# Optimization experiments

Measured on AMD Instinct MI355X. Metric: run time of the kernel, lower is better.

The kernel has to match this reference:

```python
import jax, jax.numpy as jnp
import numpy as np


def setup_inputs() -> dict:
    key = jax.random.key(0)
    ks = jax.random.split(key, 5)
    B, C, H, W = 4, 256, 48, 48
    x = jax.random.normal(ks[0], (B, C, H, W), dtype=jnp.float32)
    w_qkv = jax.random.normal(ks[1], (3 * C, C), dtype=jnp.float32) * (C ** -0.5)
    b_qkv = jax.random.normal(ks[2], (3 * C,), dtype=jnp.float32) * 0.02
    w_proj = jax.random.normal(ks[3], (C, C), dtype=jnp.float32) * (C ** -0.5)
    b_proj = jax.random.normal(ks[4], (C,), dtype=jnp.float32) * 0.02
    return {"x": x, "w_qkv": w_qkv, "b_qkv": b_qkv, "w_proj": w_proj, "b_proj": b_proj, "num_heads": 4}


def reference(x, w_qkv, b_qkv, w_proj, b_proj, num_heads):
    B, C, H, W = x.shape
    N = H * W
    hd = C // num_heads
    # NOTE: original uses full-dim scale, not head_dim
    scale = C ** -0.5
    # 1x1 conv == channel matmul
    qkv = jnp.einsum('bchw,oc->bohw', x, w_qkv) + b_qkv[None, :, None, None]
    qkv = qkv.reshape(B, 3, num_heads, hd, N)
    q = qkv[:, 0].transpose(0, 1, 3, 2)  # [B, h, N, d]
    k = qkv[:, 1]                         # [B, h, d, N]
    v = qkv[:, 2].transpose(0, 1, 3, 2)  # [B, h, N, d]
    attn = jax.nn.softmax((q @ k) * scale, axis=-1)  # [B, h, N, N]
    out = attn @ v                        # [B, h, N, d]
    out = out.transpose(0, 1, 3, 2).reshape(B, C, H, W)
    return jnp.einsum('bchw,oc->bohw', out, w_proj) + b_proj[None, :, None, None]
```

## Files before the change

kernel.cpp:

```cpp
#include <hip/hip_runtime.h>
#include <hip/hip_bf16.h>
#include <stdint.h>

typedef unsigned short u16;
typedef unsigned int u32;
typedef __attribute__((ext_vector_type(8))) short bf16x8;
typedef __attribute__((ext_vector_type(4))) short bf16x4;
typedef __attribute__((ext_vector_type(4))) float f32x4;
typedef __attribute__((ext_vector_type(2))) unsigned int u32x2;
typedef __attribute__((ext_vector_type(4))) unsigned short u16x4;

#define MFMA16 __builtin_amdgcn_mfma_f32_16x16x32_bf16

#if __has_builtin(__builtin_amdgcn_mfma_f32_16x16x16bf16_1k)
__device__ __forceinline__ f32x4 MFMAK16(u32x2 a, u32x2 b, f32x4 c) {
  return __builtin_amdgcn_mfma_f32_16x16x16bf16_1k(
      __builtin_bit_cast(bf16x4, a), __builtin_bit_cast(bf16x4, b), c, 0, 0, 0);
}
#elif __has_builtin(__builtin_amdgcn_mfma_f32_16x16x16_bf16)
typedef __attribute__((ext_vector_type(4))) __bf16 bf16v4;
__device__ __forceinline__ f32x4 MFMAK16(u32x2 a, u32x2 b, f32x4 c) {
  return __builtin_amdgcn_mfma_f32_16x16x16_bf16(
      __builtin_bit_cast(bf16v4, a), __builtin_bit_cast(bf16v4, b), c, 0, 0, 0);
}
#else
__device__ __forceinline__ f32x4 MFMAK16(u32x2 a, u32x2 b, f32x4 c) {
  f32x4 d;
  asm("s_nop 1\n\tv_mfma_f32_16x16x16_bf16 %0, %1, %2, %3"
      : "=v"(d) : "v"(a), "v"(b), "v"(c));
  return d;
}
#endif

static constexpr int Bb = 4;
static constexpr int Cc = 256;
static constexpr int NHh = 4;
static constexpr int HDd = 64;
static constexpr int Nn = 2304;
static constexpr int NSPLIT = 6;

__device__ __forceinline__ u16 f2bf(float f) {
  u32 u = __builtin_bit_cast(u32, f);
  u32 r = u + 0x7fffu + ((u >> 16) & 1u);
  return (u16)(r >> 16);
}

__device__ __forceinline__ u32 cvtpk(float a, float b) {
  u32 r;
  asm("v_cvt_pk_bf16_f32 %0, %1, %2" : "=v"(r) : "v"(a), "v"(b));
  return r;
}

__device__ __forceinline__ float blo(u32 u) { return __builtin_bit_cast(float, u << 16); }
__device__ __forceinline__ float bhi(u32 u) { return __builtin_bit_cast(float, u & 0xffff0000u); }

__device__ __forceinline__ void async16(const void* g, void* l) {
  __builtin_amdgcn_global_load_lds(
      (const __attribute__((address_space(1))) u32*)g,
      (__attribute__((address_space(3))) u32*)l, 16, 0, 0);
}

__global__ __launch_bounds__(256) void k_prep(const float* __restrict__ wq,
                                              const float* __restrict__ wp,
                                              u16* __restrict__ wqb,
                                              u16* __restrict__ wpb) {
  int i = blockIdx.x * 256 + threadIdx.x;
  if (i < 3 * Cc * Cc) wqb[i] = f2bf(wq[i]);
  if (i < Cc * Cc)     wpb[i] = f2bf(wp[i]);
}

__global__ __launch_bounds__(256) void k_qkv(const u16* __restrict__ wqb,
                                             const float* __restrict__ x,
                                             const float* __restrict__ bqkv,
                                             u16* __restrict__ qT, u16* __restrict__ kT,
                                             u16* __restrict__ vT) {
  __shared__ float tile[64][65];
  __shared__ u16 Bs[64 * 256];
  int n0 = blockIdx.y * 64, b = blockIdx.z;
  int t = threadIdx.x, w = t >> 6, l = t & 63, g = l >> 4, li = l & 15;
  char* BsB = (char*)Bs;
#pragma unroll
  for (int cc = 0; cc < 4; ++cc) {
#pragma unroll
    for (int i = 0; i < 16; ++i) {
      int cl = i * 4 + w;
      tile[cl][l] = x[((size_t)(b * Cc + cc * 64 + cl)) * Nn + n0 + l];
    }
    __syncthreads();
#pragma unroll
    for (int i = 0; i < 16; ++i) {
      int nr = i * 4 + w;
      int byte = nr * 512 + ((2 * (cc * 64 + l)) ^ ((nr & 7) << 4));
      *(u16*)(BsB + byte) = f2bf(tile[l][nr]);
    }
    __syncthreads();
  }
  const float qs = 0.0625f * 1.44269504088896340736f;
#pragma unroll
  for (int p = 0; p < 2; ++p) {
    int o0 = blockIdx.x * 128 + p * 64;
    const u16* Arow = wqb + (size_t)(o0 + w * 16 + li) * Cc;
    f32x4 acc[4] = {};
#pragma unroll
    for (int s = 0; s < 8; ++s) {
      bf16x8 a = *(const bf16x8*)(Arow + s * 32 + g * 8);
#pragma unroll
      for (int nt = 0; nt < 4; ++nt) {
        int row = nt * 16 + li;
        const char* bp_ = (const char*)Bs + row * 512 + ((s * 64 + g * 16) ^ ((row & 7) << 4));
        bf16x8 bb = *(const bf16x8*)bp_;
        acc[nt] = MFMA16(a, bb, acc[nt], 0, 0, 0);
      }
    }
    int which = o0 >> 8;
    int hh = (o0 >> 6) & 3;
    int bh = b * NHh + hh;
    int dbase = w * 16 + g * 4;
#pragma unroll
    for (int nt = 0; nt < 4; ++nt) {
      int n = n0 + nt * 16 + li;
      float v0 = acc[nt][0] + bqkv[o0 + dbase + 0];
      float v1 = acc[nt][1] + bqkv[o0 + dbase + 1];
      float v2 = acc[nt][2] + bqkv[o0 + dbase + 2];
      float v3 = acc[nt][3] + bqkv[o0 + dbase + 3];
      if (which == 0) {
        u16x4 pq = {f2bf(v0 * qs), f2bf(v1 * qs), f2bf(v2 * qs), f2bf(v3 * qs)};
        *(u16x4*)(qT + ((size_t)bh * Nn + n) * HDd + dbase) = pq;
      } else if (which == 1) {
        u16x4 pk = {f2bf(v0), f2bf(v1), f2bf(v2), f2bf(v3)};
        *(u16x4*)(kT + ((size_t)bh * Nn + n) * HDd + dbase) = pk;
      } else {
        vT[((size_t)bh * HDd + dbase + 0) * Nn + n] = f2bf(v0);
        vT[((size_t)bh * HDd + dbase + 1) * Nn + n] = f2bf(v1);
        vT[((size_t)bh * HDd + dbase + 2) * Nn + n] = f2bf(v2);
        vT[((size_t)bh * HDd + dbase + 3) * Nn + n] = f2bf(v3);
      }
    }
  }
}

__global__ __launch_bounds__(192) void k_attn(const u16* __restrict__ qT,
                                              const u16* __restrict__ kT,
                                              const u16* __restrict__ vT,
                                              u16* __restrict__ attP,
                                              float* __restrict__ lsumP) {
  __shared__ u16 Ks[2][32 * 64];
  __shared__ u16 Vs[2][64 * 32];
  int L = blockIdx.x;
  int xcd = L & 7, r2 = L >> 3;
  int bh = 2 * xcd + (r2 >= 144 ? 1 : 0);
  int rr = (r2 >= 144) ? r2 - 144 : r2;
  int sext = rr / 24;
  int qb = rr % 24;
  int t = threadIdx.x, w = t / 64, l = t & 63, g = l >> 4, li = l & 15;
  int q0 = qb * 96 + w * 32;
  const u16* qr0 = qT + ((size_t)bh * Nn + q0 + li) * HDd;
  const u16* qr1 = qT + ((size_t)bh * Nn + q0 + 16 + li) * HDd;
  bf16x8 bq[2][2];
  bq[0][0] = *(const bf16x8*)(qr0 + g * 8);
  bq[0][1] = *(const bf16x8*)(qr0 + 32 + g * 8);
  bq[1][0] = *(const bf16x8*)(qr1 + g * 8);
  bq[1][1] = *(const bf16x8*)(qr1 + 32 + g * 8);
  const u32 one2 = 0x3F803F80u;
  u32x2 ONESK = {one2, one2};
  f32x4 acc[2][4] = {};
  f32x4 acc_l[2] = {};
  const char* kbh = (const char*)(kT + (size_t)bh * Nn * HDd);
  const char* vbh = (const char*)(vT + (size_t)bh * HDd * Nn);
  int sw_li = (li & 7) << 4;
  int sw2   = ((li >> 1) & 3) << 4;

  const char* sp[3];
  int sd[3];
  ptrdiff_t sstr[3];
  bool son[3], svv[3];
#pragma unroll
  for (int it = 0; it < 3; ++it) {
    int gg = w * 3 + it;
    son[it] = (gg < 8);
    int c = gg * 64 + l;
    if (c < 256) {
      int key = c >> 3, c8 = c & 7;
      sp[it] = kbh + (size_t)(sext * 384 + key) * 128 + ((c8 * 16) ^ ((key & 7) << 4));
      sd[it] = c * 16; sstr[it] = 32 * 128; svv[it] = false;
    } else {
      int cv = c - 256, d = cv >> 2, c4 = cv & 3;
      sp[it] = vbh + (size_t)d * (Nn * 2) + sext * 768 +
               ((c4 * 16) ^ (((d >> 1) & 3) << 4));
      sd[it] = cv * 16; sstr[it] = 32 * 2; svv[it] = true;
    }
  }

  auto STAGE = [&](int buf) {
    char* kdst = (char*)(&Ks[0][0]) + buf * 4096;
    char* vdst = (char*)(&Vs[0][0]) + buf * 4096;
#pragma unroll
    for (int it = 0; it < 3; ++it) {
      if (son[it]) {
        async16(sp[it], (svv[it] ? vdst : kdst) + sd[it]);
        sp[it] += sstr[it];
      }
    }
  };

  STAGE(0);
  int cur = 0;
  for (int kb = 0; kb < 12; ++kb) {
    __syncthreads();
    if (kb + 1 < 12) STAGE(cur ^ 1);

    const char* Kc = (const char*)(&Ks[0][0]) + cur * 4096;
    const char* Vc = (const char*)(&Vs[0][0]) + cur * 4096;

    f32x4 s[2][2];
    __builtin_amdgcn_s_setprio(1);
#pragma unroll
    for (int kt = 0; kt < 2; ++kt) {
      const char* kr = Kc + (kt * 16 + li) * 128;
      bf16x8 a0 = *(const bf16x8*)(kr + ((g * 16) ^ sw_li));
      bf16x8 a1 = *(const bf16x8*)(kr + ((64 + g * 16) ^ sw_li));
#pragma unroll
      for (int st = 0; st < 2; ++st) {
        f32x4 z = {};
        z = MFMA16(a0, bq[st][0], z, 0, 0, 0);
        z = MFMA16(a1, bq[st][1], z, 0, 0, 0);
        s[st][kt] = z;
      }
    }
    __builtin_amdgcn_s_setprio(0);

    u32x2 pb[2][2];
#pragma unroll
    for (int st = 0; st < 2; ++st)
#pragma unroll
      for (int kt = 0; kt < 2; ++kt) {
#pragma unroll
        for (int j = 0; j < 4; ++j) s[st][kt][j] = exp2f(s[st][kt][j]);
        pb[st][kt][0] = cvtpk(s[st][kt][0], s[st][kt][1]);
        pb[st][kt][1] = cvtpk(s[st][kt][2], s[st][kt][3]);
      }

    __builtin_amdgcn_s_setprio(1);
    acc_l[0] = MFMAK16(ONESK, pb[0][0], acc_l[0]);
    acc_l[0] = MFMAK16(ONESK, pb[0][1], acc_l[0]);
    acc_l[1] = MFMAK16(ONESK, pb[1][0], acc_l[1]);
    acc_l[1] = MFMAK16(ONESK, pb[1][1], acc_l[1]);
#pragma unroll
    for (int dt = 0; dt < 4; ++dt) {
      const char* vr = Vc + (dt * 16 + li) * 64;
#pragma unroll
      for (int kt = 0; kt < 2; ++kt) {
        u32x2 vf = *(const u32x2*)(vr + ((kt * 32 + g * 8) ^ sw2));
        acc[0][dt] = MFMAK16(vf, pb[0][kt], acc[0][dt]);
        acc[1][dt] = MFMAK16(vf, pb[1][kt], acc[1][dt]);
      }
    }
    __builtin_amdgcn_s_setprio(0);
    cur ^= 1;
  }
  asm volatile("s_nop 7\n\ts_nop 7");
  u16* ap = attP + (size_t)sext * (Bb * Nn * Cc);
  float* lp = lsumP + sext * (Bb * NHh * Nn);
  if (l < 16) {
    lp[bh * Nn + q0 + li] = acc_l[0][0];
    lp[bh * Nn + q0 + 16 + li] = acc_l[1][0];
  }
  int b = bh >> 2, hh = bh & 3;
#pragma unroll
  for (int st = 0; st < 2; ++st) {
    int q = q0 + st * 16 + li;
#pragma unroll
    for (int dt = 0; dt < 4; ++dt) {
      u16x4 pk = {f2bf(acc[st][dt][0]), f2bf(acc[st][dt][1]),
                  f2bf(acc[st][dt][2]), f2bf(acc[st][dt][3])};
      *(u16x4*)(ap + ((size_t)(b * Nn + q)) * Cc + hh * 64 + dt * 16 + g * 4) = pk;
    }
  }
}

__global__ __launch_bounds__(256) void k_merge(const u16* __restrict__ attP,
                                               const float* __restrict__ lsumP,
                                               u16* __restrict__ attT) {
  int gid = blockIdx.x * 256 + threadIdx.x;
  int base = gid * 8;
  int bidx = base / (Nn * Cc);
  int rem = base - bidx * (Nn * Cc);
  int n = rem >> 8, c = rem & 255;
  int hh = c >> 6;
  int lidx = (bidx * NHh + hh) * Nn + n;
  const int LQ = Bb * NHh * Nn;
  float lsum = 0.f;
#pragma unroll
  for (int q = 0; q < NSPLIT; ++q) lsum += lsumP[q * LQ + lidx];
  float inv = 1.0f / lsum;
  const size_t QSZ = (size_t)Bb * Nn * Cc;
  float s0 = 0, s1 = 0, s2 = 0, s3 = 0, s4 = 0, s5 = 0, s6 = 0, s7 = 0;
#pragma unroll
  for (int q = 0; q < NSPLIT; ++q) {
    uint4 p = *(const uint4*)(attP + q * QSZ + base);
    s0 += blo(p.x); s1 += bhi(p.x);
    s2 += blo(p.y); s3 += bhi(p.y);
    s4 += blo(p.z); s5 += bhi(p.z);
    s6 += blo(p.w); s7 += bhi(p.w);
  }
  uint4 o;
  o.x = cvtpk(s0 * inv, s1 * inv);
  o.y = cvtpk(s2 * inv, s3 * inv);
  o.z = cvtpk(s4 * inv, s5 * inv);
  o.w = cvtpk(s6 * inv, s7 * inv);
  *(uint4*)(attT + base) = o;
}

__global__ __launch_bounds__(256) void k_proj(const u16* __restrict__ wpb,
                                              const u16* __restrict__ attT,
                                              const float* __restrict__ bp,
                                              float* __restrict__ out) {
  __shared__ u16 Bs[32 * 256];
  int bx = blockIdx.x, n0 = blockIdx.y * 32, b = blockIdx.z;
  int t = threadIdx.x, w = t >> 6, l = t & 63, g = l >> 4, li = l & 15;
#pragma unroll
  for (int it = 0; it < 4; ++it) {
    int ch = it * 256 + t;
    int row = ch >> 5, c16 = ch & 31;
    const char* src = (const char*)attT + ((size_t)(b * Nn + n0 + row)) * 512 +
                      ((c16 * 16) ^ ((row & 7) << 4));
    async16(src, (char*)Bs + (it * 256 + (t & ~63)) * 16);
  }
  const u16* Arow0 = wpb + (size_t)(bx * 128 + w * 16 + li) * Cc;
  const u16* Arow1 = Arow0 + (size_t)64 * Cc;
  __syncthreads();
  f32x4 acc[2][2] = {};
#pragma unroll
  for (int s = 0; s < 8; ++s) {
    bf16x8 a0 = *(const bf16x8*)(Arow0 + s * 32 + g * 8);
    bf16x8 a1 = *(const bf16x8*)(Arow1 + s * 32 + g * 8);
#pragma unroll
    for (int nt = 0; nt < 2; ++nt) {
      int row = nt * 16 + li;
      const char* bp_ = (const char*)Bs + row * 512 + ((s * 64 + g * 16) ^ ((row & 7) << 4));
      bf16x8 bb = *(const bf16x8*)bp_;
      acc[0][nt] = MFMA16(a0, bb, acc[0][nt], 0, 0, 0);
      acc[1][nt] = MFMA16(a1, bb, acc[1][nt], 0, 0, 0);
    }
  }
#pragma unroll
  for (int nt = 0; nt < 2; ++nt) {
    int n = n0 + nt * 16 + li;
#pragma unroll
    for (int p = 0; p < 2; ++p) {
      int obase = bx * 128 + p * 64 + w * 16 + g * 4;
#pragma unroll
      for (int j = 0; j < 4; ++j) {
        out[((size_t)(b * Cc + obase + j)) * Nn + n] = acc[p][nt][j] + bp[obase + j];
      }
    }
  }
}

extern "C" void kernel_launch(void* const* d_in, const int* in_sizes, int n_in,
                              void* d_out, int out_size, void* d_ws, size_t ws_size,
                              hipStream_t stream) {
  const float* x     = (const float*)d_in[0];
  const float* wqkv  = (const float*)d_in[1];
  const float* bqkv  = (const float*)d_in[2];
  const float* wproj = (const float*)d_in[3];
  const float* bproj = (const float*)d_in[4];
  float* out = (float*)d_out;

  u16* ws    = (u16*)d_ws;
  u16* wq_bf = ws;
  u16* wp_bf = wq_bf + 196608;
  u16* qT    = wp_bf + 65536;
  u16* kT    = qT + 2359296;
  u16* vT    = kT + 2359296;
  u16* attP  = vT + 2359296;
  float* lsumP = (float*)(attP + NSPLIT * 2359296);
  u16* attT  = qT;

  k_prep<<<dim3(768), dim3(256), 0, stream>>>(wqkv, wproj, wq_bf, wp_bf);
  k_qkv<<<dim3(6, 36, 4), dim3(256), 0, stream>>>(wq_bf, x, bqkv, qT, kT, vT);
  k_attn<<<dim3(2304), dim3(192), 0, stream>>>(qT, kT, vT, attP, lsumP);
  k_merge<<<dim3(1152), dim3(256), 0, stream>>>(attP, lsumP, attT);
  k_proj<<<dim3(2, 72, 4), dim3(256), 0, stream>>>(wp_bf, attT, bproj, out);
}
```

Measured before the change: 90.72 us.

## Halve key-split count and double attention key tile to 64 keys

Splits each head's keys into 3 chunks instead of 6 and stages 64-key K/V tiles per iteration instead of 32, with a new V swizzle. This halves the number of attention blocks, the partial-output writes, and the merge traffic, and each block does more MFMA work per barrier. The costs are doubled LDS use per block, more registers for the larger P tile, and fewer blocks in flight, which may reduce occupancy and latency hiding.

```diff
diff --git a/kernel.cpp b/kernel.cpp
--- a/kernel.cpp
+++ b/kernel.cpp
@@ -37,7 +37,7 @@
 static constexpr int NHh = 4;
 static constexpr int HDd = 64;
 static constexpr int Nn = 2304;
-static constexpr int NSPLIT = 6;
+static constexpr int NSPLIT = 3;
 
 __device__ __forceinline__ u16 f2bf(float f) {
   u32 u = __builtin_bit_cast(u32, f);
@@ -144,12 +144,12 @@
                                               const u16* __restrict__ vT,
                                               u16* __restrict__ attP,
                                               float* __restrict__ lsumP) {
-  __shared__ u16 Ks[2][32 * 64];
-  __shared__ u16 Vs[2][64 * 32];
+  __shared__ u16 Ks[2][64 * 64];
+  __shared__ u16 Vs[2][64 * 64];
   int L = blockIdx.x;
   int xcd = L & 7, r2 = L >> 3;
-  int bh = 2 * xcd + (r2 >= 144 ? 1 : 0);
-  int rr = (r2 >= 144) ? r2 - 144 : r2;
+  int bh = 2 * xcd + (r2 >= 72 ? 1 : 0);
+  int rr = (r2 >= 72) ? r2 - 72 : r2;
   int sext = rr / 24;
   int qb = rr % 24;
   int t = threadIdx.x, w = t / 64, l = t & 63, g = l >> 4, li = l & 15;
@@ -168,34 +168,33 @@
   const char* kbh = (const char*)(kT + (size_t)bh * Nn * HDd);
   const char* vbh = (const char*)(vT + (size_t)bh * HDd * Nn);
   int sw_li = (li & 7) << 4;
-  int sw2   = ((li >> 1) & 3) << 4;
-
-  const char* sp[3];
-  int sd[3];
-  ptrdiff_t sstr[3];
-  bool son[3], svv[3];
-#pragma unroll
-  for (int it = 0; it < 3; ++it) {
-    int gg = w * 3 + it;
-    son[it] = (gg < 8);
+
+  const char* sp[6];
+  int sd[6];
+  ptrdiff_t sstr[6];
+  bool son[6], svv[6];
+#pragma unroll
+  for (int it = 0; it < 6; ++it) {
+    int gg = w * 6 + it;
+    son[it] = (gg < 16);
     int c = gg * 64 + l;
-    if (c < 256) {
+    if (c < 512) {
       int key = c >> 3, c8 = c & 7;
-      sp[it] = kbh + (size_t)(sext * 384 + key) * 128 + ((c8 * 16) ^ ((key & 7) << 4));
-      sd[it] = c * 16; sstr[it] = 32 * 128; svv[it] = false;
+      sp[it] = kbh + (size_t)(sext * 768 + key) * 128 + ((c8 * 16) ^ ((key & 7) << 4));
+      sd[it] = c * 16; sstr[it] = 64 * 128; svv[it] = false;
     } else {
-      int cv = c - 256, d = cv >> 2, c4 = cv & 3;
-      sp[it] = vbh + (size_t)d * (Nn * 2) + sext * 768 +
-               ((c4 * 16) ^ (((d >> 1) & 3) << 4));
-      sd[it] = cv * 16; sstr[it] = 32 * 2; svv[it] = true;
+      int cv = c - 512, d = cv >> 3, c8 = cv & 7;
+      sp[it] = vbh + (size_t)d * (Nn * 2) + (size_t)(sext * 768) * 2 +
+               ((c8 * 16) ^ ((d & 7) << 4));
+      sd[it] = cv * 16; sstr[it] = 64 * 2; svv[it] = true;
     }
   }
 
   auto STAGE = [&](int buf) {
-    char* kdst = (char*)(&Ks[0][0]) + buf * 4096;
-    char* vdst = (char*)(&Vs[0][0]) + buf * 4096;
-#pragma unroll
-    for (int it = 0; it < 3; ++it) {
+    char* kdst = (char*)(&Ks[0][0]) + buf * 8192;
+    char* vdst = (char*)(&Vs[0][0]) + buf * 8192;
+#pragma unroll
+    for (int it = 0; it < 6; ++it) {
       if (son[it]) {
         async16(sp[it], (svv[it] ? vdst : kdst) + sd[it]);
         sp[it] += sstr[it];
@@ -209,50 +208,48 @@
     __syncthreads();
     if (kb + 1 < 12) STAGE(cur ^ 1);
 
-    const char* Kc = (const char*)(&Ks[0][0]) + cur * 4096;
-    const char* Vc = (const char*)(&Vs[0][0]) + cur * 4096;
-
-    f32x4 s[2][2];
-    __builtin_amdgcn_s_setprio(1);
-#pragma unroll
-    for (int kt = 0; kt < 2; ++kt) {
-      const char* kr = Kc + (kt * 16 + li) * 128;
-      bf16x8 a0 = *(const bf16x8*)(kr + ((g * 16) ^ sw_li));
-      bf16x8 a1 = *(const bf16x8*)(kr + ((64 + g * 16) ^ sw_li));
-#pragma unroll
-      for (int st = 0; st < 2; ++st) {
+    const char* Kc = (const char*)(&Ks[0][0]) + cur * 8192;
+    const char* Vc = (const char*)(&Vs[0][0]) + cur * 8192;
+
+    u32x2 pb[2][4];
+#pragma unroll
+    for (int st = 0; st < 2; ++st) {
+      f32x4 s[4];
+      __builtin_amdgcn_s_setprio(1);
+#pragma unroll
+      for (int kt = 0; kt < 4; ++kt) {
+        const char* kr = Kc + (kt * 16 + li) * 128;
+        bf16x8 a0 = *(const bf16x8*)(kr + ((g * 16) ^ sw_li));
+        bf16x8 a1 = *(const bf16x8*)(kr + ((64 + g * 16) ^ sw_li));
         f32x4 z = {};
         z = MFMA16(a0, bq[st][0], z, 0, 0, 0);
         z = MFMA16(a1, bq[st][1], z, 0, 0, 0);
-        s[st][kt] = z;
-      }
-    }
-    __builtin_amdgcn_s_setprio(0);
-
-    u32x2 pb[2][2];
-#pragma unroll
-    for (int st = 0; st < 2; ++st)
-#pragma unroll
-      for (int kt = 0; kt < 2; ++kt) {
-#pragma unroll
-        for (int j = 0; j < 4; ++j) s[st][kt][j] = exp2f(s[st][kt][j]);
-        pb[st][kt][0] = cvtpk(s[st][kt][0], s[st][kt][1]);
-        pb[st][kt][1] = cvtpk(s[st][kt][2], s[st][kt][3]);
-      }
+        s[kt] = z;
+      }
+      __builtin_amdgcn_s_setprio(0);
+#pragma unroll
+      for (int kt = 0; kt < 4; ++kt) {
+#pragma unroll
+        for (int j = 0; j < 4; ++j) s[kt][j] = exp2f(s[kt][j]);
+        pb[st][kt][0] = cvtpk(s[kt][0], s[kt][1]);
+        pb[st][kt][1] = cvtpk(s[kt][2], s[kt][3]);
+      }
+    }
 
     __builtin_amdgcn_s_setprio(1);
-    acc_l[0] = MFMAK16(ONESK, pb[0][0], acc_l[0]);
-    acc_l[0] = MFMAK16(ONESK, pb[0][1], acc_l[0]);
-    acc_l[1] = MFMAK16(ONESK, pb[1][0], acc_l[1]);
-    acc_l[1] = MFMAK16(ONESK, pb[1][1], acc_l[1]);
+#pragma unroll
+    for (int ktg = 0; ktg < 4; ++ktg) {
+      acc_l[0] = MFMAK16(ONESK, pb[0][ktg], acc_l[0]);
+      acc_l[1] = MFMAK16(ONESK, pb[1][ktg], acc_l[1]);
+    }
 #pragma unroll
     for (int dt = 0; dt < 4; ++dt) {
-      const char* vr = Vc + (dt * 16 + li) * 64;
-#pragma unroll
-      for (int kt = 0; kt < 2; ++kt) {
-        u32x2 vf = *(const u32x2*)(vr + ((kt * 32 + g * 8) ^ sw2));
-        acc[0][dt] = MFMAK16(vf, pb[0][kt], acc[0][dt]);
-        acc[1][dt] = MFMAK16(vf, pb[1][kt], acc[1][dt]);
+      const char* vr = Vc + (dt * 16 + li) * 128;
+#pragma unroll
+      for (int ktg = 0; ktg < 4; ++ktg) {
+        u32x2 vf = *(const u32x2*)(vr + ((ktg * 32 + g * 8) ^ sw_li));
+        acc[0][dt] = MFMAK16(vf, pb[0][ktg], acc[0][dt]);
+        acc[1][dt] = MFMAK16(vf, pb[1][ktg], acc[1][dt]);
       }
     }
     __builtin_amdgcn_s_setprio(0);
@@ -379,7 +376,7 @@
 
   k_prep<<<dim3(768), dim3(256), 0, stream>>>(wqkv, wproj, wq_bf, wp_bf);
   k_qkv<<<dim3(6, 36, 4), dim3(256), 0, stream>>>(wq_bf, x, bqkv, qT, kT, vT);
-  k_attn<<<dim3(2304), dim3(192), 0, stream>>>(qT, kT, vT, attP, lsumP);
+  k_attn<<<dim3(1152), dim3(192), 0, stream>>>(qT, kT, vT, attP, lsumP);
   k_merge<<<dim3(1152), dim3(256), 0, stream>>>(attP, lsumP, attT);
   k_proj<<<dim3(2, 72, 4), dim3(256), 0, stream>>>(wp_bf, attT, bproj, out);
 }
```

After: 98.02 us. +8.1%, slower.
